# Kernel tuning notes

Hardware: AMD Instinct MI355X
Metric: run time of the kernel (lower is better)

Reference implementation:

```python
import jax, jax.numpy as jnp
import numpy as np

IOU_THR = 0.5
SCORE_THR = 0.5
MAX_OUT = 300  # max_output_boxes_per_batch


def setup_inputs() -> dict:
    key = jax.random.key(0)
    kb, ks = jax.random.split(key)
    B, N, C = 8, 1024, 32
    u = jax.random.uniform(kb, (B, N, 4), dtype=jnp.float32)
    ctr = u[..., :2] * 100.0          # box centers in [0,100)
    sz = u[..., 2:] * 20.0 + 1.0      # box sizes in [1,21)
    # y1x1y2x2 format (as the torch module expects)
    boxes = jnp.concatenate([ctr - 0.5 * sz, ctr + 0.5 * sz], axis=-1)
    scores = jax.random.uniform(ks, (B, N, C), dtype=jnp.float32)
    return {"boxes": boxes, "scores": scores}


def _pairwise_iou(b):
    # b: [C, N, 4] in y1x1y2x2; IoU is invariant to the axis swap so no
    # conversion to x1y1x2y2 is needed.
    y1, x1, y2, x2 = b[..., 0], b[..., 1], b[..., 2], b[..., 3]
    area = (y2 - y1) * (x2 - x1)                          # [C, N]
    yy1 = jnp.maximum(y1[..., :, None], y1[..., None, :])
    xx1 = jnp.maximum(x1[..., :, None], x1[..., None, :])
    yy2 = jnp.minimum(y2[..., :, None], y2[..., None, :])
    xx2 = jnp.minimum(x2[..., :, None], x2[..., None, :])
    inter = jnp.clip(yy2 - yy1, 0.0) * jnp.clip(xx2 - xx1, 0.0)
    return inter / (area[..., :, None] + area[..., None, :] - inter)


def _nms_keep(iou, valid, thr):
    # Sequential greedy suppression, vectorized across classes.
    # iou: [C, N, N] (score-descending order), valid: [C, N] bool.
    N = iou.shape[-1]
    idx = jnp.arange(N)

    def body(i, keep):
        sup = (iou[:, i, :] > thr) & keep[:, i][:, None] & (idx[None, :] > i)
        return keep & ~sup

    return jax.lax.fori_loop(0, N, body, valid)


def _nms_single(boxes, scores):
    # boxes: [N, 4], scores: [N, C]  ->  ([M,4], [M], [M])
    N, C = scores.shape
    M = MAX_OUT
    sc = scores.T                                  # [C, N]
    valid = sc > SCORE_THR
    s = jnp.where(valid, sc, -jnp.inf)
    order = jnp.argsort(-s, axis=1, stable=True)   # per-class score desc
    sb = boxes[order]                              # [C, N, 4]
    ss = jnp.take_along_axis(s, order, axis=1)     # [C, N]
    sv = jnp.take_along_axis(valid, order, axis=1)
    keep = _nms_keep(_pairwise_iou(sb), sv, IOU_THR)   # [C, N]

    # flatten class-major (matches torch scores.transpose(1,0).flatten())
    fb = sb.reshape(C * N, 4)
    fs = ss.reshape(-1)
    fk = keep.reshape(-1)
    fcls = jnp.repeat(jnp.arange(C, dtype=jnp.int32), N)
    fbind = order.reshape(-1)                      # original box index

    # global score-descending order over kept detections, truncate to M
    g = jnp.where(fk, fs, -jnp.inf)
    gord = jnp.argsort(-g, stable=True)[:M]
    tb, ts, tc, ti, tv = fb[gord], fs[gord], fcls[gord], fbind[gord], fk[gord]

    # dedup by original box index: keep highest-score (first) occurrence;
    # torch's _get_unique_first_indices re-orders by ascending box index.
    p = jnp.arange(M, dtype=jnp.int32)
    first = jnp.full((N,), M, dtype=jnp.int32).at[ti].min(jnp.where(tv, p, M))
    present = first < M                            # [N]
    ordN = jnp.argsort(~present, stable=True)[:M]  # present box ids, ascending
    pos = first[ordN]
    m = present[ordN]
    posc = jnp.where(m, pos, 0)
    out_boxes = jnp.where(m[:, None], tb[posc], 0.0)
    out_scores = jnp.where(m, ts[posc], 0.0)
    out_classes = jnp.where(m, tc[posc], 0)
    return out_boxes, out_scores, out_classes


def reference(boxes, scores):
    ob, osc, ocl = jax.vmap(_nms_single)(boxes, scores)
    # matches torch return (output_boxes, output_scores, output_classes)
    return ob, osc, ocl
```

## Files before the change

### kernel.cpp

```cpp
#include <hip/hip_runtime.h>

#pragma clang fp contract(off)

#define NBOX   1024
#define NCLS   32
#define NBATCH 8
#define MAXOUT 300
#define SMAX   11

#define MTHR 0x1.000001p-1

__device__ __forceinline__ unsigned long long shflx64(unsigned long long v, int m) {
  unsigned lo = (unsigned)__shfl_xor((int)(unsigned)v, m, 64);
  unsigned hi = (unsigned)__shfl_xor((int)(unsigned)(v >> 32), m, 64);
  return ((unsigned long long)hi << 32) | lo;
}

__device__ __forceinline__ unsigned long long cexch(
    unsigned long long mine, int jj, int kk, int t) {
  unsigned long long other = shflx64(mine, jj);
  bool iLow = ((t & jj) == 0);
  bool desc = ((t & kk) == 0);
  bool wantMax = (iLow == desc);
  bool otherBigger = (other > mine);
  return (wantMax == otherBigger) ? other : mine;
}

__global__ __launch_bounds__(1024) void nms_per_class(
    const float* __restrict__ boxes, const float* __restrict__ scores,
    unsigned long long* __restrict__ recs) {
#pragma clang fp contract(off)
  const int bc = blockIdx.x;
  const int b = bc >> 5;
  const int c = bc & (NCLS - 1);
  const int t = threadIdx.x;
  const int lane = t & 63, wav = t >> 6;

  __shared__ unsigned long long key[NBOX];
  __shared__ float4 sbox[NBOX];
  __shared__ float sarea[NBOX];
  __shared__ unsigned long long mask[64 * 68];
  __shared__ unsigned long long kb[2][16];
  __shared__ int chg[64];
  __shared__ int shV;

  const float* sp = scores + (size_t)b * NBOX * NCLS + c;
  float s = sp[(size_t)t * NCLS];
  bool valid = (s > 0.5f);
  unsigned long long mine = valid
      ? ((((unsigned long long)__float_as_uint(s)) << 32) | (unsigned)(NBOX - 1 - t))
      : (unsigned long long)(unsigned)(NBOX - 1 - t);
  if (t == 0) shV = 0;
  if (t < 64) chg[t] = 0;
  __syncthreads();
  unsigned long long vb = __ballot(valid);
  if (lane == 0) atomicAdd(&shV, (int)__popcll(vb));

  for (int kk = 2; kk <= 64; kk <<= 1)
    for (int jj = kk >> 1; jj > 0; jj >>= 1)
      mine = cexch(mine, jj, kk, t);
  key[t] = mine;
  __syncthreads();
  for (int kk = 128; kk <= 1024; kk <<= 1) {
    for (int jj = kk >> 1; jj >= 64; jj >>= 1) {
      if (t < 512) {
        int i = ((t & ~(jj - 1)) << 1) | (t & (jj - 1));
        int ixj = i | jj;
        unsigned long long a = key[i], bb = key[ixj];
        if (((i & kk) == 0) ? (a < bb) : (a > bb)) { key[i] = bb; key[ixj] = a; }
      }
      __syncthreads();
    }
    mine = key[t];
    for (int jj = 32; jj > 0; jj >>= 1) mine = cexch(mine, jj, kk, t);
    key[t] = mine;
    __syncthreads();
  }

  int n0 = NBOX - 1 - (int)(mine & (NBOX - 1));
  const float4* gb = (const float4*)boxes + (size_t)b * NBOX;
  float4 bx4 = gb[n0];
  sbox[t] = bx4;
  sarea[t] = (bx4.z - bx4.x) * (bx4.w - bx4.y);
  __syncthreads();
  const int V = shV;
  const int S = (V + 63) >> 6;
  const bool aj = (t < V);

  if (t < 16) {
    int base = t * 64;
    unsigned long long m0;
    if (V >= base + 64) m0 = ~0ull;
    else if (V <= base) m0 = 0ull;
    else m0 = (1ull << (V - base)) - 1ull;
    kb[0][t] = m0;
  }

  unsigned long long m[16];
#pragma unroll
  for (int w = 0; w < 16; ++w) m[w] = 0;

  if (S <= SMAX) {
    const int T = S * (S + 1) / 2;
    for (int k = wav; k < T; k += 16) {
      int J = 0;
      while ((J + 1) * (J + 2) / 2 <= k) ++J;
      int I = k - J * (J + 1) / 2;
      const int j = (J << 6) + lane;
      const float4 bj = sbox[j];
      const float areaj = sarea[j];
      const float4* bi = &sbox[I << 6];
      const float* ai = &sarea[I << 6];
      unsigned long long acc = 0;
#pragma unroll
      for (int q = 0; q < 64; ++q) {
        float4 a = bi[q];
        float aa = ai[q];
        float yy1 = fmaxf(a.x, bj.x);
        float xx1 = fmaxf(a.y, bj.y);
        float yy2 = fminf(a.z, bj.z);
        float xx2 = fminf(a.w, bj.w);
        float ih = fmaxf(yy2 - yy1, 0.0f);
        float iw = fmaxf(xx2 - xx1, 0.0f);
        float inter = ih * iw;
        float denom = (aa + areaj) - inter;
        if ((double)inter > MTHR * (double)denom) acc |= (1ull << q);
      }
      if (I == J) acc &= (1ull << lane) - 1ull;
      int vrem = V - (I << 6);
      if (vrem < 64) acc &= (1ull << vrem) - 1ull;
      mask[((J * (J + 1) / 2) << 6) + lane * (J + 1) + I] = acc;
    }
    __syncthreads();
    if (t < (S << 6)) {
      const int J = t >> 6;
      const int rb = ((J * (J + 1) / 2) << 6) + lane * (J + 1);
#pragma unroll
      for (int I = 0; I < 16; ++I)
        if (I <= J) m[I] = mask[rb + I];
    }
    __syncthreads();
  } else {
    const int J = t >> 6;
    const float4 bj = sbox[t];
    const float areaj = sarea[t];
#pragma unroll
    for (int I = 0; I < 16; ++I) {
      unsigned long long acc = 0;
      if (I <= J && (I << 6) < V) {
        for (int q = 0; q < 64; ++q) {
          int i = (I << 6) + q;
          float4 a = sbox[i];
          float aa = sarea[i];
          float yy1 = fmaxf(a.x, bj.x);
          float xx1 = fmaxf(a.y, bj.y);
          float yy2 = fminf(a.z, bj.z);
          float xx2 = fminf(a.w, bj.w);
          float ih = fmaxf(yy2 - yy1, 0.0f);
          float iw = fmaxf(xx2 - xx1, 0.0f);
          float inter = ih * iw;
          float denom = (aa + areaj) - inter;
          bool pred = (i < t) && (i < V) &&
                      ((double)inter > MTHR * (double)denom);
          if (pred) acc |= (1ull << q);
        }
      }
      m[I] = acc;
    }
    __syncthreads();
  }

  int cur = 0;
  for (int it = 0; it < 1100; ++it) {
    bool sup = false;
#pragma unroll
    for (int w = 0; w < 16; ++w) sup = sup || ((m[w] & kb[cur][w]) != 0ull);
    unsigned long long nb = __ballot(aj && !sup);
    if (lane == 0) {
      kb[cur ^ 1][wav] = nb;
      if (nb != kb[cur][wav]) atomicOr(&chg[it & 63], 1);
    }
    if (t == 0) chg[(it + 32) & 63] = 0;
    __syncthreads();
    if (chg[it & 63] == 0) break;
    cur ^= 1;
  }

  int tot = 0;
#pragma unroll
  for (int w = 0; w < 16; ++w) tot += (int)__popcll(kb[cur][w]);
  const int rbase = bc * MAXOUT;
  if (aj && ((kb[cur][wav] >> lane) & 1ull)) {
    int rank = 0;
#pragma unroll
    for (int w = 0; w < 16; ++w)
      if (w < wav) rank += (int)__popcll(kb[cur][w]);
    rank += (int)__popcll(kb[cur][wav] & ((1ull << lane) - 1ull));
    if (rank < MAXOUT) {
      unsigned sbits = (unsigned)(mine >> 32);
      int n = NBOX - 1 - (int)(mine & (NBOX - 1));
      int flat = c * NBOX + t;
      recs[rbase + rank] = (((unsigned long long)sbits) << 32)
          | ((unsigned)(NCLS * NBOX - 1 - flat) << 10) | (unsigned)n;
    }
  }
  if (t < MAXOUT && t >= tot) recs[rbase + t] = 0ull;
}

__global__ __launch_bounds__(1024) void topk_out(
    const float* __restrict__ boxes,
    const unsigned long long* __restrict__ recs,
    float* __restrict__ out) {
  const int b = blockIdx.x;
  const int tid = threadIdx.x;
  const int lane = tid & 63, wav = tid >> 6;

  __shared__ int hist[256];
  __shared__ int suf[257];
  __shared__ unsigned long long maxKey[NBOX];
  __shared__ unsigned long long blist[1024];
  __shared__ int bcnt;
  __shared__ unsigned long long shT;
  __shared__ int shBstar;
  __shared__ int wcnt[16], woff[16];
  __shared__ int shPresTot;

  const int CAND = NCLS * MAXOUT;
  const unsigned long long* rb = recs + (size_t)b * NCLS * MAXOUT;
  unsigned long long cand[10];
#pragma unroll
  for (int q = 0; q < 10; ++q) {
    int j = tid + (q << 10);
    cand[q] = (j < CAND) ? rb[j] : 0ull;
  }
  maxKey[tid] = 0;
  if (tid < 256) hist[tid] = 0;
  if (tid == 0) { bcnt = 0; shT = 0; shBstar = -1; }
  __syncthreads();

#pragma unroll
  for (int q = 0; q < 10; ++q) {
    unsigned long long v = cand[q];
    if (v != 0ull) {
      int bk = (int)(((unsigned)(v >> 32) - 0x3F000000u) >> 15);
      atomicAdd(&hist[bk], 1);
    }
  }
  __syncthreads();

  if (wav == 0) {
    int h[4];
#pragma unroll
    for (int g = 0; g < 4; ++g) h[g] = hist[g * 64 + lane];
#pragma unroll
    for (int g = 0; g < 4; ++g) {
      int v = h[g];
#pragma unroll
      for (int off = 1; off < 64; off <<= 1) {
        int u = __shfl_down(v, off);
        if (lane + off < 64) v += u;
      }
      h[g] = v;
    }
    int sum1 = __shfl(h[1], 0);
    int sum2 = __shfl(h[2], 0);
    int sum3 = __shfl(h[3], 0);
    suf[0 * 64 + lane] = h[0] + sum1 + sum2 + sum3;
    suf[1 * 64 + lane] = h[1] + sum2 + sum3;
    suf[2 * 64 + lane] = h[2] + sum3;
    suf[3 * 64 + lane] = h[3];
    if (lane == 0) suf[256] = 0;
  }
  __syncthreads();

  if (tid < 256) {
    if (suf[tid] >= MAXOUT && suf[tid + 1] < MAXOUT) shBstar = tid;
  }
  __syncthreads();
  const int Bstar = shBstar;

  if (Bstar >= 0) {
#pragma unroll
    for (int q = 0; q < 10; ++q) {
      unsigned long long v = cand[q];
      if (v != 0ull) {
        int bk = (int)(((unsigned)(v >> 32) - 0x3F000000u) >> 15);
        if (bk == Bstar) { int idx = atomicAdd(&bcnt, 1); blist[idx] = v; }
      }
    }
    __syncthreads();
    int M = bcnt;
    int need = MAXOUT - suf[Bstar + 1];
    if (tid < M) {
      unsigned long long mine = blist[tid];
      int r = 0;
      for (int i = 0; i < M; ++i) r += (blist[i] > mine) ? 1 : 0;
      if (r == need - 1) shT = mine;
    }
    __syncthreads();
  }
  const unsigned long long T = shT;

#pragma unroll
  for (int q = 0; q < 10; ++q) {
    unsigned long long v = cand[q];
    if (v != 0ull && v >= T) {
      int n = (int)(v & (NBOX - 1));
      atomicMax(&maxKey[n], v);
    }
  }
  __syncthreads();

  bool pres = (maxKey[tid] != 0ull);
  unsigned long long wm = __ballot(pres);
  if (lane == 0) wcnt[wav] = (int)__popcll(wm);
  __syncthreads();
  if (tid < 16) {
    int v = wcnt[tid];
    int inc = v;
#pragma unroll
    for (int off = 1; off < 16; off <<= 1) {
      int u = __shfl_up(inc, off);
      if (lane >= off) inc += u;
    }
    woff[tid] = inc - v;
    if (tid == 15) shPresTot = inc;
  }
  __syncthreads();
  const int total = shPresTot;

  float* ob = out + (size_t)b * MAXOUT * 4;
  float* os = out + (size_t)NBATCH * MAXOUT * 4 + (size_t)b * MAXOUT;
  float* oc = out + (size_t)NBATCH * MAXOUT * 5 + (size_t)b * MAXOUT;

  if (pres) {
    int slot = woff[wav] + (int)__popcll(wm & ((1ull << lane) - 1ull));
    unsigned long long v = maxKey[tid];
    float score = __uint_as_float((unsigned)(v >> 32));
    int flat = NCLS * NBOX - 1 - (int)((v >> 10) & (unsigned)(NCLS * NBOX - 1));
    int cls = flat >> 10;
    float4 bx = ((const float4*)boxes)[(size_t)b * NBOX + tid];
    ob[slot * 4 + 0] = bx.x;
    ob[slot * 4 + 1] = bx.y;
    ob[slot * 4 + 2] = bx.z;
    ob[slot * 4 + 3] = bx.w;
    os[slot] = score;
    oc[slot] = (float)cls;
  }
  if (tid >= total && tid < MAXOUT) {
    ob[tid * 4 + 0] = 0.0f; ob[tid * 4 + 1] = 0.0f;
    ob[tid * 4 + 2] = 0.0f; ob[tid * 4 + 3] = 0.0f;
    os[tid] = 0.0f;
    oc[tid] = 0.0f;
  }
}

extern "C" void kernel_launch(void* const* d_in, const int* in_sizes, int n_in,
                              void* d_out, int out_size, void* d_ws, size_t ws_size,
                              hipStream_t stream) {
  const float* boxes  = (const float*)d_in[0];
  const float* scores = (const float*)d_in[1];
  float* out = (float*)d_out;

  unsigned long long* recs = (unsigned long long*)d_ws;

  nms_per_class<<<NBATCH * NCLS, 1024, 0, stream>>>(boxes, scores, recs);
  topk_out<<<NBATCH, 1024, 0, stream>>>(boxes, recs, out);
}
```

Baseline: 103.0 us.

## Restructure NMS mask build, wave-sequential suppression, float IoU test, per-wave histograms

Replaces the double-precision IoU threshold compare with an equivalent float form (2*inter - denom > denom*2^-24), and computes three column blocks per wave work item so each row box load is reused three times. The block-wide fixed-point suppression loop, which needed a barrier per iteration, becomes a wave-by-wave pass where each wave resolves its own diagonal block with ballots and then publishes its keep mask. In the top-k kernel, shared-memory histogram atomics are spread over per-wave copies and summed afterwards. These changes aim to cut FP64 work, barrier count and atomic contention, at the cost of more registers, an extra reduction step and a suppression pass that now runs serially across waves.

```diff
diff --git a/kernel.cpp b/kernel.cpp
--- a/kernel.cpp
+++ b/kernel.cpp
@@ -8,7 +8,19 @@
 #define MAXOUT 300
 #define SMAX   11
 
-#define MTHR 0x1.000001p-1
+#define IOU_SUP(ab, aa, bj, arj, act, acc) do {               \
+    float yy1 = fmaxf((ab).x, (bj).x);                        \
+    float xx1 = fmaxf((ab).y, (bj).y);                        \
+    float yy2 = fminf((ab).z, (bj).z);                        \
+    float xx2 = fminf((ab).w, (bj).w);                        \
+    float ih = fmaxf(yy2 - yy1, 0.0f);                        \
+    float iw = fmaxf(xx2 - xx1, 0.0f);                        \
+    float inter = ih * iw;                                    \
+    float denom = ((aa) + (arj)) - inter;                     \
+    float lhs = (inter + inter) - denom;                      \
+    float rhs = denom * 5.9604644775390625e-08f;              \
+    if ((act) && (lhs > rhs)) (acc) |= bit;                   \
+  } while (0)
 
 __device__ __forceinline__ unsigned long long shflx64(unsigned long long v, int m) {
   unsigned lo = (unsigned)__shfl_xor((int)(unsigned)v, m, 64);
@@ -40,8 +52,7 @@
   __shared__ float4 sbox[NBOX];
   __shared__ float sarea[NBOX];
   __shared__ unsigned long long mask[64 * 68];
-  __shared__ unsigned long long kb[2][16];
-  __shared__ int chg[64];
+  __shared__ unsigned long long kb[16];
   __shared__ int shV;
 
   const float* sp = scores + (size_t)b * NBOX * NCLS + c;
@@ -51,7 +62,7 @@
       ? ((((unsigned long long)__float_as_uint(s)) << 32) | (unsigned)(NBOX - 1 - t))
       : (unsigned long long)(unsigned)(NBOX - 1 - t);
   if (t == 0) shV = 0;
-  if (t < 64) chg[t] = 0;
+  if (t < 16) kb[t] = 0ull;
   __syncthreads();
   unsigned long long vb = __ballot(valid);
   if (lane == 0) atomicAdd(&shV, (int)__popcll(vb));
@@ -87,115 +98,118 @@
   const int S = (V + 63) >> 6;
   const bool aj = (t < V);
 
-  if (t < 16) {
-    int base = t * 64;
-    unsigned long long m0;
-    if (V >= base + 64) m0 = ~0ull;
-    else if (V <= base) m0 = 0ull;
-    else m0 = (1ull << (V - base)) - 1ull;
-    kb[0][t] = m0;
-  }
-
-  unsigned long long m[16];
-#pragma unroll
-  for (int w = 0; w < 16; ++w) m[w] = 0;
+  unsigned long long mext[15];
+  unsigned long long mself = 0ull;
+#pragma unroll
+  for (int w = 0; w < 15; ++w) mext[w] = 0ull;
 
   if (S <= SMAX) {
-    const int T = S * (S + 1) / 2;
-    for (int k = wav; k < T; k += 16) {
-      int J = 0;
-      while ((J + 1) * (J + 2) / 2 <= k) ++J;
-      int I = k - J * (J + 1) / 2;
-      const int j = (J << 6) + lane;
-      const float4 bj = sbox[j];
-      const float areaj = sarea[j];
+    int NC = 0;
+    for (int I2 = 0; I2 < S; ++I2) NC += (S - I2 + 2) / 3;
+    for (int k = wav; k < NC; k += 16) {
+      int I = 0, rem = k;
+      for (;;) { int cI = (S - I + 2) / 3; if (rem < cI) break; rem -= cI; ++I; }
+      const int J0 = I + 3 * rem;
+      const bool h1 = (J0 + 1 < S), h2 = (J0 + 2 < S);
+      const int j0 = (J0 << 6) + lane;
+      const int j1 = h1 ? j0 + 64 : j0;
+      const int j2 = h2 ? j0 + 128 : j0;
+      const float4 b0 = sbox[j0]; const float ar0 = sarea[j0];
+      const float4 b1 = sbox[j1]; const float ar1 = sarea[j1];
+      const float4 b2 = sbox[j2]; const float ar2 = sarea[j2];
+      const bool act0 = (j0 < V);
+      const bool act1 = h1 && (j0 + 64 < V);
+      const bool act2 = h2 && (j0 + 128 < V);
       const float4* bi = &sbox[I << 6];
       const float* ai = &sarea[I << 6];
-      unsigned long long acc = 0;
-#pragma unroll
+      unsigned long long a0 = 0, a1 = 0, a2 = 0;
+      unsigned long long bit = 1ull;
+#pragma unroll 8
       for (int q = 0; q < 64; ++q) {
-        float4 a = bi[q];
+        float4 ab = bi[q];
         float aa = ai[q];
-        float yy1 = fmaxf(a.x, bj.x);
-        float xx1 = fmaxf(a.y, bj.y);
-        float yy2 = fminf(a.z, bj.z);
-        float xx2 = fminf(a.w, bj.w);
-        float ih = fmaxf(yy2 - yy1, 0.0f);
-        float iw = fmaxf(xx2 - xx1, 0.0f);
-        float inter = ih * iw;
-        float denom = (aa + areaj) - inter;
-        if ((double)inter > MTHR * (double)denom) acc |= (1ull << q);
-      }
-      if (I == J) acc &= (1ull << lane) - 1ull;
-      int vrem = V - (I << 6);
-      if (vrem < 64) acc &= (1ull << vrem) - 1ull;
-      mask[((J * (J + 1) / 2) << 6) + lane * (J + 1) + I] = acc;
+        IOU_SUP(ab, aa, b0, ar0, act0, a0);
+        IOU_SUP(ab, aa, b1, ar1, act1, a1);
+        IOU_SUP(ab, aa, b2, ar2, act2, a2);
+        bit <<= 1;
+      }
+      if (rem == 0) a0 &= (1ull << lane) - 1ull;
+      const int vrem = V - (I << 6);
+      if (vrem < 64) {
+        unsigned long long tm = (1ull << vrem) - 1ull;
+        a0 &= tm; a1 &= tm; a2 &= tm;
+      }
+      mask[(((J0 * (J0 + 1) / 2) << 6) + lane * (J0 + 1)) + I] = a0;
+      if (h1) mask[((((J0 + 1) * (J0 + 2) / 2) << 6) + lane * (J0 + 2)) + I] = a1;
+      if (h2) mask[((((J0 + 2) * (J0 + 3) / 2) << 6) + lane * (J0 + 3)) + I] = a2;
     }
     __syncthreads();
     if (t < (S << 6)) {
-      const int J = t >> 6;
-      const int rb = ((J * (J + 1) / 2) << 6) + lane * (J + 1);
-#pragma unroll
-      for (int I = 0; I < 16; ++I)
-        if (I <= J) m[I] = mask[rb + I];
-    }
-    __syncthreads();
+      const int J = wav;
+      const int rbs = ((J * (J + 1) / 2) << 6) + lane * (J + 1);
+#pragma unroll
+      for (int I = 0; I < 15; ++I)
+        if (I < J) mext[I] = mask[rbs + I];
+      mself = mask[rbs + J];
+    }
   } else {
-    const int J = t >> 6;
+    const int J = wav;
     const float4 bj = sbox[t];
-    const float areaj = sarea[t];
+    const float arj = sarea[t];
 #pragma unroll
     for (int I = 0; I < 16; ++I) {
-      unsigned long long acc = 0;
       if (I <= J && (I << 6) < V) {
+        unsigned long long acc = 0, bit = 1ull;
         for (int q = 0; q < 64; ++q) {
           int i = (I << 6) + q;
-          float4 a = sbox[i];
+          float4 ab = sbox[i];
           float aa = sarea[i];
-          float yy1 = fmaxf(a.x, bj.x);
-          float xx1 = fmaxf(a.y, bj.y);
-          float yy2 = fminf(a.z, bj.z);
-          float xx2 = fminf(a.w, bj.w);
-          float ih = fmaxf(yy2 - yy1, 0.0f);
-          float iw = fmaxf(xx2 - xx1, 0.0f);
-          float inter = ih * iw;
-          float denom = (aa + areaj) - inter;
-          bool pred = (i < t) && (i < V) &&
-                      ((double)inter > MTHR * (double)denom);
-          if (pred) acc |= (1ull << q);
+          bool act = aj && (i < t) && (i < V);
+          IOU_SUP(ab, aa, bj, arj, act, acc);
+          bit <<= 1;
         }
-      }
-      m[I] = acc;
-    }
-    __syncthreads();
-  }
-
-  int cur = 0;
-  for (int it = 0; it < 1100; ++it) {
-    bool sup = false;
-#pragma unroll
-    for (int w = 0; w < 16; ++w) sup = sup || ((m[w] & kb[cur][w]) != 0ull);
-    unsigned long long nb = __ballot(aj && !sup);
-    if (lane == 0) {
-      kb[cur ^ 1][wav] = nb;
-      if (nb != kb[cur][wav]) atomicOr(&chg[it & 63], 1);
-    }
-    if (t == 0) chg[(it + 32) & 63] = 0;
-    __syncthreads();
-    if (chg[it & 63] == 0) break;
-    cur ^= 1;
-  }
-
+        if (I == J) mself = acc;
+        else mext[I] = acc;
+      }
+    }
+  }
+  __syncthreads();
+
+  const int NW = S;
+  for (int w = 0; w < NW; ++w) {
+    if (wav == w) {
+      bool supExt = false;
+#pragma unroll
+      for (int i = 0; i < 15; ++i)
+        if (i < w) supExt = supExt || ((mext[i] & kb[i]) != 0ull);
+      bool alive = aj && !supExt;
+      unsigned long long cur = __ballot(alive);
+      for (;;) {
+        unsigned long long nb = __ballot(alive && ((mself & cur) == 0ull));
+        if (nb == cur) break;
+        cur = nb;
+      }
+      if (lane == 0) kb[w] = cur;
+    }
+    __syncthreads();
+  }
+
+  unsigned long long kbr[16];
+#pragma unroll
+  for (int w = 0; w < 16; ++w) kbr[w] = kb[w];
   int tot = 0;
 #pragma unroll
-  for (int w = 0; w < 16; ++w) tot += (int)__popcll(kb[cur][w]);
+  for (int w = 0; w < 16; ++w) tot += (int)__popcll(kbr[w]);
   const int rbase = bc * MAXOUT;
-  if (aj && ((kb[cur][wav] >> lane) & 1ull)) {
+  unsigned long long kw = kbr[0];
+#pragma unroll
+  for (int w = 1; w < 16; ++w) if (w == wav) kw = kbr[w];
+  if (aj && ((kw >> lane) & 1ull)) {
     int rank = 0;
 #pragma unroll
     for (int w = 0; w < 16; ++w)
-      if (w < wav) rank += (int)__popcll(kb[cur][w]);
-    rank += (int)__popcll(kb[cur][wav] & ((1ull << lane) - 1ull));
+      if (w < wav) rank += (int)__popcll(kbr[w]);
+    rank += (int)__popcll(kw & ((1ull << lane) - 1ull));
     if (rank < MAXOUT) {
       unsigned sbits = (unsigned)(mine >> 32);
       int n = NBOX - 1 - (int)(mine & (NBOX - 1));
@@ -215,6 +229,7 @@
   const int tid = threadIdx.x;
   const int lane = tid & 63, wav = tid >> 6;
 
+  __shared__ int histw[16 * 256];
   __shared__ int hist[256];
   __shared__ int suf[257];
   __shared__ unsigned long long maxKey[NBOX];
@@ -234,7 +249,8 @@
     cand[q] = (j < CAND) ? rb[j] : 0ull;
   }
   maxKey[tid] = 0;
-  if (tid < 256) hist[tid] = 0;
+#pragma unroll
+  for (int q = 0; q < 4; ++q) histw[tid + (q << 10)] = 0;
   if (tid == 0) { bcnt = 0; shT = 0; shBstar = -1; }
   __syncthreads();
 
@@ -243,8 +259,15 @@
     unsigned long long v = cand[q];
     if (v != 0ull) {
       int bk = (int)(((unsigned)(v >> 32) - 0x3F000000u) >> 15);
-      atomicAdd(&hist[bk], 1);
-    }
+      atomicAdd(&histw[(wav << 8) + bk], 1);
+    }
+  }
+  __syncthreads();
+  if (tid < 256) {
+    int ssum = 0;
+#pragma unroll
+    for (int w = 0; w < 16; ++w) ssum += histw[(w << 8) + tid];
+    hist[tid] = ssum;
   }
   __syncthreads();
 
```

New measurement: 102.5 us. Within noise of the previous version (-0.5%).
